# Kernel tuning notes

Hardware: AMD Instinct MI355X
Metric: run time of the kernel (lower is better)

Reference implementation:

```python
import jax, jax.numpy as jnp
import numpy as np

NEG_SLOPE = 0.2

def _gatv2(x_src, x_dst, src, dst, Wl, bl, Wr, br, att, bias, num_dst, edge_feat=None, We=None):
    # PyG GATv2Conv (heads=1, add_self_loops=False, eval mode -> no dropout)
    xl = x_src @ Wl + bl                      # [Ns, C] lin_l on source
    xr = x_dst @ Wr + br                      # [Nd, C] lin_r on target
    m = xl[src] + xr[dst]                     # [E, C]
    if edge_feat is not None:
        m = m + edge_feat @ We                # lin_edge (bias=False)
    e = jax.nn.leaky_relu(m, NEG_SLOPE) @ att # [E] attention logits
    emax = jax.ops.segment_max(e, dst, num_segments=num_dst)
    ee = jnp.exp(e - emax[dst])
    denom = jax.ops.segment_sum(ee, dst, num_segments=num_dst)
    alpha = ee / jnp.maximum(denom[dst], 1e-16)
    out = jax.ops.segment_sum(alpha[:, None] * xl[src], dst, num_segments=num_dst)
    return out + bias


def setup_inputs() -> dict:
    key = jax.random.key(0)
    N_OP, N_M, N_A = 50000, 5000, 2000
    C_OP, C_M, C_A = 256, 128, 128
    E_OO, E_OM, E_MA, E_DIM = 200000, 200000, 60000, 8
    ks = jax.random.split(key, 40)
    i = iter(range(40))
    def nrm(shape, fan_in):
        return jax.random.normal(ks[next(i)], shape, dtype=jnp.float32) / np.sqrt(fan_in)
    inp = {}
    inp['x_op'] = jax.random.normal(ks[next(i)], (N_OP, C_OP), dtype=jnp.float32)
    inp['x_m'] = jax.random.normal(ks[next(i)], (N_M, C_M), dtype=jnp.float32)
    inp['x_a'] = jax.random.normal(ks[next(i)], (N_A, C_A), dtype=jnp.float32)
    inp['ei_pred'] = jax.random.randint(ks[next(i)], (2, E_OO), 0, N_OP)
    inp['ei_succ'] = jax.random.randint(ks[next(i)], (2, E_OO), 0, N_OP)
    inp['src_o2m'] = jax.random.randint(ks[next(i)], (E_OM,), 0, N_OP)
    inp['dst_o2m'] = jax.random.randint(ks[next(i)], (E_OM,), 0, N_M)
    inp['src_m2a'] = jax.random.randint(ks[next(i)], (E_MA,), 0, N_M)
    inp['dst_m2a'] = jax.random.randint(ks[next(i)], (E_MA,), 0, N_A)
    inp['ea_m2a'] = jax.random.normal(ks[next(i)], (E_MA, E_DIM), dtype=jnp.float32)
    for name, c_in_src, c_in_dst, c_out in [('pred', C_OP, C_OP, C_OP), ('succ', C_OP, C_OP, C_OP), ('o2m', C_OP, C_M, C_M), ('m2a', C_M, C_A, C_A)]:
        inp[f'Wl_{name}'] = nrm((c_in_src, c_out), c_in_src)
        inp[f'bl_{name}'] = jnp.zeros((c_out,), jnp.float32)
        inp[f'Wr_{name}'] = nrm((c_in_dst, c_out), c_in_dst)
        inp[f'br_{name}'] = jnp.zeros((c_out,), jnp.float32)
        inp[f'att_{name}'] = nrm((c_out,), c_out)
        inp[f'b_{name}'] = jnp.zeros((c_out,), jnp.float32)
    inp['We_m2a'] = nrm((E_DIM, C_A), E_DIM)
    return inp


def reference(x_op, x_m, x_a, ei_pred, ei_succ, src_o2m, dst_o2m, src_m2a, dst_m2a, ea_m2a,
              Wl_pred, bl_pred, Wr_pred, br_pred, att_pred, b_pred,
              Wl_succ, bl_succ, Wr_succ, br_succ, att_succ, b_succ,
              Wl_o2m, bl_o2m, Wr_o2m, br_o2m, att_o2m, b_o2m,
              Wl_m2a, bl_m2a, Wr_m2a, br_m2a, att_m2a, b_m2a, We_m2a):
    N_OP, N_M, N_A = x_op.shape[0], x_m.shape[0], x_a.shape[0]
    # operation_relation_extract: two op->op GATv2 convs, HeteroConv sum-aggregated
    f_pred = _gatv2(x_op, x_op, ei_pred[0], ei_pred[1], Wl_pred, bl_pred, Wr_pred, br_pred, att_pred, b_pred, N_OP)
    f_succ = _gatv2(x_op, x_op, ei_succ[0], ei_succ[1], Wl_succ, bl_succ, Wr_succ, br_succ, att_succ, b_succ, N_OP)
    # hetero_relation_extract
    f_mach = _gatv2(x_op, x_m, src_o2m, dst_o2m, Wl_o2m, bl_o2m, Wr_o2m, br_o2m, att_o2m, b_o2m, N_M)
    f_agv = _gatv2(x_m, x_a, src_m2a, dst_m2a, Wl_m2a, bl_m2a, Wr_m2a, br_m2a, att_m2a, b_m2a, N_A, edge_feat=ea_m2a, We=We_m2a)
    # residual sum across relation outputs per node type
    out_op = x_op + f_pred + f_succ
    out_m = x_m + f_mach
    out_a = x_a + f_agv
    return (out_op, out_m, out_a)
```

## Files before the change

### kernel.cpp

```cpp
#include <hip/hip_runtime.h>

#define N_OP   50000
#define N_M    5000
#define N_A    2000
#define C_OP   256
#define C_M    128
#define C_A    128
#define E_OO   200000
#define E_OM   200000
#define E_MA   60000
#define E_DIM  8

#define OUT_OP_OFF 0
#define OUT_M_OFF  (N_OP * C_OP)
#define OUT_A_OFF  (N_OP * C_OP + N_M * C_M)

typedef short bf16x8 __attribute__((ext_vector_type(8)));
typedef float f32x4 __attribute__((ext_vector_type(4)));
typedef __attribute__((address_space(1))) const unsigned gu32;
typedef __attribute__((address_space(3))) unsigned lu32;

__device__ __forceinline__ unsigned short f2bf(float f) {
    unsigned u = __float_as_uint(f);
    unsigned r = (u + 0x7FFFu + ((u >> 16) & 1u)) >> 16;
    return (unsigned short)r;
}
__device__ __forceinline__ float bf2f(unsigned short h) {
    return __uint_as_float(((unsigned)h) << 16);
}

#define NTOT 107000
#define ETOT 660000

#define I3_OP (N_OP * C_OP / 4)
#define I3_M  (I3_OP + N_M * C_M / 4)
#define I3_A  (I3_M + N_A * C_A / 4)

#define PK_P   131072
#define PK_S   262144
#define PK_OL  294912
#define PK_OR  311296
#define PK_ML  327680
#define PK_MR  344064
#define PK_BP  344576
#define PK_BS  345088

#define PREP_HIST_BLK ((ETOT + 255) / 256)
#define PREP_INIT_BLK (I3_A / 256)
#define PREP_PACK_BLK (PK_BS / 256)
#define PREP_TOTAL    (PREP_HIST_BLK + PREP_INIT_BLK + PREP_PACK_BLK)

__device__ __forceinline__ void init_one(const float* __restrict__ x,
                                         const float* __restrict__ b1,
                                         const float* __restrict__ b2,
                                         float* __restrict__ out,
                                         unsigned short* __restrict__ xc,
                                         int i, int cmask) {
    float4 v = ((const float4*)x)[i];
    const int cb = i & cmask;
    float4 b = ((const float4*)b1)[cb];
    if (b2) {
        float4 t = ((const float4*)b2)[cb];
        b.x += t.x; b.y += t.y; b.z += t.z; b.w += t.w;
    }
    float4 o;
    o.x = v.x + b.x; o.y = v.y + b.y; o.z = v.z + b.z; o.w = v.w + b.w;
    ((float4*)out)[i] = o;
    ushort4 r;
    r.x = f2bf(v.x); r.y = f2bf(v.y); r.z = f2bf(v.z); r.w = f2bf(v.w);
    ((ushort4*)xc)[i] = r;
}

__global__ void prep_all(
    const int* __restrict__ dP, const int* __restrict__ dS,
    const int* __restrict__ dO, const int* __restrict__ dA,
    int* __restrict__ cP, int* __restrict__ cS,
    int* __restrict__ cO, int* __restrict__ cA, int* __restrict__ rk,
    const float* __restrict__ x_op, const float* __restrict__ x_m,
    const float* __restrict__ x_a,
    const float* __restrict__ bP, const float* __restrict__ bS,
    const float* __restrict__ bO, const float* __restrict__ bA,
    float* __restrict__ out_op, float* __restrict__ out_m, float* __restrict__ out_a,
    unsigned short* __restrict__ xcop, unsigned short* __restrict__ xcm,
    unsigned short* __restrict__ xca,
    const float* __restrict__ WlP, const float* __restrict__ WrP,
    const float* __restrict__ WlS, const float* __restrict__ WrS,
    const float* __restrict__ WOl, const float* __restrict__ WOr,
    const float* __restrict__ WMl, const float* __restrict__ WMr,
    const float* __restrict__ blP, const float* __restrict__ brP,
    const float* __restrict__ blS, const float* __restrict__ brS,
    unsigned short* __restrict__ BtP, unsigned short* __restrict__ BtS,
    unsigned short* __restrict__ BtOL, unsigned short* __restrict__ BtOR,
    unsigned short* __restrict__ BtML, unsigned short* __restrict__ BtMR,
    float* __restrict__ biasP, float* __restrict__ biasS) {
    const int b = blockIdx.x;
    const int tid = threadIdx.x;
    if (b < PREP_HIST_BLK) {
        int i = b * 256 + tid;
        if (i < 200000)      rk[i] = atomicAdd(&cP[dP[i]], 1);
        else if (i < 400000) rk[i] = atomicAdd(&cS[dS[i - 200000]], 1);
        else if (i < 600000) rk[i] = atomicAdd(&cO[dO[i - 400000]], 1);
        else if (i < ETOT)   rk[i] = atomicAdd(&cA[dA[i - 600000]], 1);
    } else if (b < PREP_HIST_BLK + PREP_INIT_BLK) {
        int i = (b - PREP_HIST_BLK) * 256 + tid;
        if (i < I3_OP)      init_one(x_op, bP, bS, out_op, xcop, i, 63);
        else if (i < I3_M)  init_one(x_m, bO, nullptr, out_m, xcm, i - I3_OP, 31);
        else                init_one(x_a, bA, nullptr, out_a, xca, i - I3_M, 31);
    } else {
        int i = (b - PREP_HIST_BLK - PREP_INIT_BLK) * 256 + tid;
        if (i < PK_P) {
            int n = i >> 8, k = i & 255;
            BtP[i] = f2bf((n < 256) ? WlP[k * 256 + n] : WrP[k * 256 + (n - 256)]);
        } else if (i < PK_S) {
            int j = i - PK_P; int n = j >> 8, k = j & 255;
            BtS[j] = f2bf((n < 256) ? WlS[k * 256 + n] : WrS[k * 256 + (n - 256)]);
        } else if (i < PK_OL) {
            int j = i - PK_S; int n = j >> 8, k = j & 255;
            BtOL[j] = f2bf(WOl[k * 128 + n]);
        } else if (i < PK_OR) {
            int j = i - PK_OL; int n = j >> 7, k = j & 127;
            BtOR[j] = f2bf(WOr[k * 128 + n]);
        } else if (i < PK_ML) {
            int j = i - PK_OR; int n = j >> 7, k = j & 127;
            BtML[j] = f2bf(WMl[k * 128 + n]);
        } else if (i < PK_MR) {
            int j = i - PK_ML; int n = j >> 7, k = j & 127;
            BtMR[j] = f2bf(WMr[k * 128 + n]);
        } else if (i < PK_BP) {
            int j = i - PK_MR;
            biasP[j] = (j < 256) ? blP[j] : brP[j - 256];
        } else if (i < PK_BS) {
            int j = i - PK_BP;
            biasS[j] = (j < 256) ? blS[j] : brS[j - 256];
        }
    }
}

__device__ __forceinline__ void gload_lds16(const void* g, void* l) {
    __builtin_amdgcn_global_load_lds((gu32*)g, (lu32*)l, 16, 0, 0);
}

__device__ __forceinline__ void gemm_body(
    const unsigned short* __restrict__ A, const unsigned short* __restrict__ Bt,
    const float* __restrict__ bias, unsigned short* __restrict__ C,
    int M, int K, int ldc, int bx, int by,
    unsigned short (&As)[2][128 * 64], unsigned short (&Bs)[2][128 * 64]) {
    const int tid  = threadIdx.x;
    const int lane = tid & 63;
    const int wid  = tid >> 6;
    const int m0   = bx * 128;
    const int n0   = by * 128;

    f32x4 acc[4][4] = {};

    const int srow   = tid >> 3;
    const int scolb  = (tid & 7) * 16;
    const int scole  = (scolb ^ ((srow & 7) << 4)) >> 1;

    int grA[4], grB[4];
#pragma unroll
    for (int i = 0; i < 4; ++i) {
        int gr = m0 + i * 32 + srow;
        grA[i] = (gr < M) ? gr : M - 1;
        grB[i] = n0 + i * 32 + srow;
    }

    const int nt = K >> 6;
    int cur = 0;

#define STAGE(buf, k0)                                                          \
    {                                                                           \
        _Pragma("unroll")                                                       \
        for (int i = 0; i < 4; ++i)                                             \
            gload_lds16(A + (size_t)grA[i] * K + (k0) + scole,                  \
                        &As[buf][i * 2048 + tid * 8]);                          \
        _Pragma("unroll")                                                       \
        for (int i = 0; i < 4; ++i)                                             \
            gload_lds16(Bt + (size_t)grB[i] * K + (k0) + scole,                 \
                        &Bs[buf][i * 2048 + tid * 8]);                          \
    }

    STAGE(0, 0)
    asm volatile("s_waitcnt vmcnt(0)" ::: "memory");
    __syncthreads();

    const int wr = (wid >> 1) * 64;
    const int wc = (wid & 1) * 64;

    for (int t = 0; t < nt; ++t) {
        if (t + 1 < nt) STAGE(cur ^ 1, (t + 1) * 64)
#pragma unroll
        for (int kh = 0; kh < 2; ++kh) {
            const int kob = kh * 64 + (lane >> 4) * 16;
            bf16x8 a[4], b[4];
#pragma unroll
            for (int mi = 0; mi < 4; ++mi) {
                const int row = wr + mi * 16 + (lane & 15);
                a[mi] = *(const bf16x8*)((const char*)As[cur] + row * 128 +
                                         (kob ^ ((row & 7) << 4)));
            }
#pragma unroll
            for (int ni = 0; ni < 4; ++ni) {
                const int row = wc + ni * 16 + (lane & 15);
                b[ni] = *(const bf16x8*)((const char*)Bs[cur] + row * 128 +
                                         (kob ^ ((row & 7) << 4)));
            }
#pragma unroll
            for (int mi = 0; mi < 4; ++mi)
#pragma unroll
                for (int ni = 0; ni < 4; ++ni)
                    acc[mi][ni] = __builtin_amdgcn_mfma_f32_16x16x32_bf16(
                        a[mi], b[ni], acc[mi][ni], 0, 0, 0);
        }
        asm volatile("s_waitcnt vmcnt(0)" ::: "memory");
        __syncthreads();
        cur ^= 1;
    }
#undef STAGE

    const int crow = (lane >> 4) * 4;
    const int ccol = lane & 15;
    float bcol[4];
#pragma unroll
    for (int ni = 0; ni < 4; ++ni) bcol[ni] = bias[n0 + wc + ni * 16 + ccol];
#pragma unroll
    for (int mi = 0; mi < 4; ++mi) {
#pragma unroll
        for (int j = 0; j < 4; ++j) {
            const int row = m0 + wr + mi * 16 + crow + j;
            if (row < M) {
                unsigned short* pc = C + (size_t)row * ldc + n0 + wc + ccol;
#pragma unroll
                for (int ni = 0; ni < 4; ++ni)
                    pc[ni * 16] = f2bf(acc[mi][ni][j] + bcol[ni]);
            }
        }
    }
}

__global__ __launch_bounds__(256) void mfma_gemm(
    const unsigned short* __restrict__ A, const unsigned short* __restrict__ Bt,
    const float* __restrict__ bias, unsigned short* __restrict__ C,
    int M, int K, int ldc) {
    __shared__ unsigned short As[2][128 * 64];
    __shared__ unsigned short Bs[2][128 * 64];
    gemm_body(A, Bt, bias, C, M, K, ldc, blockIdx.x, blockIdx.y, As, Bs);
}

#define SCAT_XBLK 645
__global__ __launch_bounds__(256) void gemm_scat(
    const unsigned short* __restrict__ A, const unsigned short* __restrict__ Bt,
    const float* __restrict__ bias, unsigned short* __restrict__ C,
    int M, int K, int ldc, int mt,
    const int* __restrict__ sP, const int* __restrict__ dP,
    const int* __restrict__ sS, const int* __restrict__ dS,
    const int* __restrict__ sO, const int* __restrict__ dO,
    const int* __restrict__ sA, const int* __restrict__ dA,
    const int* __restrict__ pP, const int* __restrict__ pS,
    const int* __restrict__ pO, const int* __restrict__ pA,
    const int* __restrict__ rk,
    int* __restrict__ srP, int* __restrict__ srS,
    int* __restrict__ srO, int* __restrict__ srA, int* __restrict__ eiA) {
    __shared__ unsigned short As[2][128 * 64];
    __shared__ unsigned short Bs[2][128 * 64];
    if ((int)blockIdx.x < mt) {
        gemm_body(A, Bt, bias, C, M, K, ldc, blockIdx.x, blockIdx.y, As, Bs);
    } else {
        const int i = (((int)blockIdx.x - mt) * 4 + (int)blockIdx.y) * 256 + (int)threadIdx.x;
        if (i < 200000) {
            srP[pP[dP[i]] + rk[i]] = sP[i];
        } else if (i < 400000) {
            const int j = i - 200000;
            srS[pS[dS[j]] + rk[i]] = sS[j];
        } else if (i < 600000) {
            const int j = i - 400000;
            srO[pO[dO[j]] + rk[i]] = sO[j];
        } else if (i < ETOT) {
            const int j = i - 600000;
            const int pos = pA[dA[j]] + rk[i];
            srA[pos] = sA[j];
            eiA[pos] = j;
        }
    }
}

__global__ __launch_bounds__(256) void gemm_pair(
    const unsigned short* A1, const unsigned short* Bt1, const float* b1,
    unsigned short* C1, int M1, int K1, int l1, int n1,
    const unsigned short* A2, const unsigned short* Bt2, const float* b2,
    unsigned short* C2, int M2, int K2, int l2) {
    __shared__ unsigned short As[2][128 * 64];
    __shared__ unsigned short Bs[2][128 * 64];
    const unsigned short *A, *Bt; const float* bi; unsigned short* C;
    int M, K, ldc, bx;
    if ((int)blockIdx.x < n1) { A = A1; Bt = Bt1; bi = b1; C = C1; M = M1; K = K1; ldc = l1; bx = blockIdx.x; }
    else                      { A = A2; Bt = Bt2; bi = b2; C = C2; M = M2; K = K2; ldc = l2; bx = blockIdx.x - n1; }
    gemm_body(A, Bt, bi, C, M, K, ldc, bx, blockIdx.y, As, Bs);
}

__global__ __launch_bounds__(256) void gemm_tri(
    const unsigned short* A1, const unsigned short* Bt1, const float* b1,
    unsigned short* C1, int M1, int K1, int n1,
    const unsigned short* A2, const unsigned short* Bt2, const float* b2,
    unsigned short* C2, int M2, int K2, int n12,
    const float* __restrict__ ea, const float* __restrict__ We,
    const int* __restrict__ eid, unsigned short* __restrict__ efo) {
    __shared__ unsigned short As[2][128 * 64];
    __shared__ unsigned short Bs[2][128 * 64];
    __shared__ float Ef[8][8];
    const int b = blockIdx.x;
    if (b < n12) {
        const unsigned short *A, *Bt; const float* bi; unsigned short* C;
        int M, K, bx;
        if (b < n1) { A = A1; Bt = Bt1; bi = b1; C = C1; M = M1; K = K1; bx = b; }
        else        { A = A2; Bt = Bt2; bi = b2; C = C2; M = M2; K = K2; bx = b - n1; }
        gemm_body(A, Bt, bi, C, M, K, 128, bx, 0, As, Bs);
    } else {
        const int eb = b - n12;
        const int m0 = eb * 8;
        const int tid = threadIdx.x;
        if (tid < 64) {
            int r = tid >> 3, k = tid & 7;
            Ef[r][k] = ea[(size_t)eid[m0 + r] * 8 + k];
        }
        __syncthreads();
        const int col = tid & 127, half = tid >> 7;
        float acc[4] = {};
        for (int k = 0; k < 8; ++k) {
            const float w = We[k * 128 + col];
#pragma unroll
            for (int r = 0; r < 4; ++r) acc[r] += Ef[half * 4 + r][k] * w;
        }
#pragma unroll
        for (int r = 0; r < 4; ++r)
            efo[(size_t)(m0 + half * 4 + r) * 128 + col] = f2bf(acc[r]);
    }
}

#define NB_P 49
#define NB_S 49
#define NB_O 5
#define NB_A 2

__global__ void zero4(int* __restrict__ p, int n) {
    int i = blockIdx.x * blockDim.x + threadIdx.x;
    if (i < n) p[i] = 0;
}

__global__ void scan_blk4(const int* __restrict__ cP, const int* __restrict__ cS,
                          const int* __restrict__ cO, const int* __restrict__ cA,
                          int* __restrict__ pP, int* __restrict__ pS,
                          int* __restrict__ pO, int* __restrict__ pA,
                          int* __restrict__ bsum) {
    __shared__ int smem[1024];
    int b = blockIdx.x;
    const int* cnt; int* ptr; int n; int bo;
    if (b < NB_P)                { cnt = cP; ptr = pP; n = 50000; bo = 0; }
    else if (b < NB_P + NB_S)    { cnt = cS; ptr = pS; n = 50000; bo = 64;  b -= NB_P; }
    else if (b < NB_P + NB_S + NB_O) { cnt = cO; ptr = pO; n = 5000; bo = 128; b -= NB_P + NB_S; }
    else                         { cnt = cA; ptr = pA; n = 2000; bo = 192; b -= NB_P + NB_S + NB_O; }
    const int tid = threadIdx.x;
    const int i = b * 1024 + tid;
    const int v = (i < n) ? cnt[i] : 0;
    smem[tid] = v;
    __syncthreads();
    for (int o = 1; o < 1024; o <<= 1) {
        int t = (tid >= o) ? smem[tid - o] : 0;
        __syncthreads();
        smem[tid] += t;
        __syncthreads();
    }
    if (i < n) ptr[i] = smem[tid] - v;
    if (tid == 1023) bsum[bo + b] = smem[1023];
}

__global__ void scan_tops4(const int* __restrict__ bsum, int* __restrict__ boff,
                           int* __restrict__ pP, int* __restrict__ pS,
                           int* __restrict__ pO, int* __restrict__ pA) {
    __shared__ int smem[1024];
    const int seg = blockIdx.x;
    const int nb = (seg < 2) ? 49 : (seg == 2 ? 5 : 2);
    const int off = seg * 64;
    int* ptr_n = (seg == 0) ? pP + 50000 : (seg == 1) ? pS + 50000
               : (seg == 2) ? pO + 5000 : pA + 2000;
    const int tid = threadIdx.x;
    const int v = (tid < nb) ? bsum[off + tid] : 0;
    smem[tid] = v;
    __syncthreads();
    for (int o = 1; o < 1024; o <<= 1) {
        int t = (tid >= o) ? smem[tid - o] : 0;
        __syncthreads();
        smem[tid] += t;
        __syncthreads();
    }
    if (tid < nb) boff[off + tid] = smem[tid] - v;
    if (tid == 1023) *ptr_n = smem[1023];
}

__global__ void scan_add4(int* __restrict__ pP, int* __restrict__ pS,
                          int* __restrict__ pO, int* __restrict__ pA,
                          const int* __restrict__ boff) {
    int i = blockIdx.x * blockDim.x + threadIdx.x;
    int* ptr; int loc; int off;
    if (i < 50000)       { ptr = pP; loc = i;          off = 0; }
    else if (i < 100000) { ptr = pS; loc = i - 50000;  off = 64; }
    else if (i < 105000) { ptr = pO; loc = i - 100000; off = 128; }
    else if (i < NTOT)   { ptr = pA; loc = i - 105000; off = 192; }
    else return;
    ptr[loc] += boff[off + (loc >> 10)];
}

template <int C>
__global__ void csr_serial2(const unsigned short* __restrict__ xl, int ldl,
                            const unsigned short* __restrict__ xr, int ldr,
                            const float* __restrict__ att,
                            const int* __restrict__ ptr, const int* __restrict__ srcs,
                            float* __restrict__ out, int n) {
    const int tid = threadIdx.x;
    const int node = blockIdx.x * (blockDim.x >> 5) + (tid >> 5);
    if (node >= n) return;
    const int gl = tid & 31;
    const int beg = ptr[node], end = ptr[node + 1];
    if (beg == end) return;

    constexpr int V = C / 32;
    const int c0 = gl * V;

    float av[V], rvf[V];
    {
        const unsigned short* pr = xr + (size_t)node * ldr + c0;
        unsigned short rv[V];
        *(uint4*)rv = *(const uint4*)pr;
#pragma unroll
        for (int v4 = 0; v4 < V / 4; ++v4)
            *(float4*)(av + v4 * 4) = ((const float4*)(att + c0))[v4];
#pragma unroll
        for (int v = 0; v < V; ++v) rvf[v] = bf2f(rv[v]);
    }

    float runM = -3.0e38f, runS = 0.0f;
    float acc[V] = {};

    unsigned short lv[V];
    {
        const unsigned short* pl = xl + (size_t)srcs[beg] * ldl + c0;
        *(uint4*)lv = *(const uint4*)pl;
    }

    for (int j = beg; j < end; ++j) {
        float cf[V];
#pragma unroll
        for (int v = 0; v < V; ++v) cf[v] = bf2f(lv[v]);
        if (j + 1 < end) {
            const unsigned short* pl = xl + (size_t)srcs[j + 1] * ldl + c0;
            *(uint4*)lv = *(const uint4*)pl;
        }

        float part = 0.0f;
#pragma unroll
        for (int v = 0; v < V; ++v) {
            float m = cf[v] + rvf[v];
            m = (m >= 0.0f) ? m : 0.2f * m;
            part += m * av[v];
        }
        part += __shfl_xor(part, 1, 64);
        part += __shfl_xor(part, 2, 64);
        part += __shfl_xor(part, 4, 64);
        part += __shfl_xor(part, 8, 64);
        part += __shfl_xor(part, 16, 64);

        const float newM = fmaxf(runM, part);
        const float sc = __expf(runM - newM);
        const float e1 = __expf(part - newM);
        runS = runS * sc + e1;
        runM = newM;
#pragma unroll
        for (int v = 0; v < V; ++v) acc[v] = acc[v] * sc + e1 * cf[v];
    }

    const float inv = 1.0f / fmaxf(runS, 1e-16f);
    float* po = out + (size_t)node * C + c0;
#pragma unroll
    for (int v4 = 0; v4 < V / 4; ++v4) {
        float4 o = ((float4*)po)[v4];
        o.x += acc[v4 * 4 + 0] * inv;
        o.y += acc[v4 * 4 + 1] * inv;
        o.z += acc[v4 * 4 + 2] * inv;
        o.w += acc[v4 * 4 + 3] * inv;
        ((float4*)po)[v4] = o;
    }
}

template <int C, bool HAS_EF>
__global__ void csr_grp(const unsigned short* __restrict__ xl, int ldl,
                        const unsigned short* __restrict__ xr, int ldr,
                        const unsigned short* __restrict__ ef,
                        const float* __restrict__ att,
                        const int* __restrict__ ptr, const int* __restrict__ srcs,
                        float* __restrict__ out, int n) {
    const int node = blockIdx.x * (blockDim.x >> 6) + (threadIdx.x >> 6);
    if (node >= n) return;
    const int lane = threadIdx.x & 63;
    const int grp  = lane >> 4;
    const int sl   = lane & 15;
    const int beg = ptr[node], end = ptr[node + 1];
    if (beg == end) return;

    constexpr int W = C / 16;
    const int c0 = sl * W;

    float av[W], rvf[W];
    {
        const unsigned short* pr = xr + (size_t)node * ldr + c0;
        unsigned short rv[W];
        *(uint4*)rv = *(const uint4*)pr;
        if constexpr (W == 16) *(uint4*)(rv + 8) = *(const uint4*)(pr + 8);
#pragma unroll
        for (int v4 = 0; v4 < W / 4; ++v4)
            *(float4*)(av + v4 * 4) = ((const float4*)(att + c0))[v4];
#pragma unroll
        for (int v = 0; v < W; ++v) rvf[v] = bf2f(rv[v]);
    }

    float runM = -3.0e38f, runS = 0.0f;
    float acc[W] = {};

    for (int cb = beg; cb < end; cb += 4) {
        const int j = cb + grp;
        const bool act = (j < end);
        const int js = act ? j : end - 1;
        const int s = srcs[js];

        const unsigned short* pl = xl + (size_t)s * ldl + c0;
        unsigned short lv[W];
        *(uint4*)lv = *(const uint4*)pl;
        if constexpr (W == 16) *(uint4*)(lv + 8) = *(const uint4*)(pl + 8);
        float cf[W];
#pragma unroll
        for (int v = 0; v < W; ++v) cf[v] = bf2f(lv[v]);

        float part = 0.0f;
        if constexpr (HAS_EF) {
            unsigned short efv[W];
            const unsigned short* pe = ef + (size_t)js * C + c0;
            *(uint4*)efv = *(const uint4*)pe;
            if constexpr (W == 16) *(uint4*)(efv + 8) = *(const uint4*)(pe + 8);
#pragma unroll
            for (int v = 0; v < W; ++v) {
                float m = cf[v] + rvf[v] + bf2f(efv[v]);
                m = (m >= 0.0f) ? m : 0.2f * m;
                part += m * av[v];
            }
        } else {
#pragma unroll
            for (int v = 0; v < W; ++v) {
                float m = cf[v] + rvf[v];
                m = (m >= 0.0f) ? m : 0.2f * m;
                part += m * av[v];
            }
        }
        part += __shfl_xor(part, 1, 64);
        part += __shfl_xor(part, 2, 64);
        part += __shfl_xor(part, 4, 64);
        part += __shfl_xor(part, 8, 64);
        if (!act) part = -3.0e38f;

        float cm = fmaxf(part, __shfl_xor(part, 16, 64));
        cm = fmaxf(cm, __shfl_xor(cm, 32, 64));

        if (cm > runM) {
            const float sc = __expf(runM - cm);
            runS *= sc;
#pragma unroll
            for (int v = 0; v < W; ++v) acc[v] *= sc;
            runM = cm;
        }
        const float w = act ? __expf(part - runM) : 0.0f;
        float cs = w + __shfl_xor(w, 16, 64);
        cs += __shfl_xor(cs, 32, 64);
        runS += cs;
#pragma unroll
        for (int v = 0; v < W; ++v) acc[v] += w * cf[v];
    }

#pragma unroll
    for (int v = 0; v < W; ++v) acc[v] += __shfl_xor(acc[v], 16, 64);
#pragma unroll
    for (int v = 0; v < W; ++v) acc[v] += __shfl_xor(acc[v], 32, 64);

    const float inv = 1.0f / fmaxf(runS, 1e-16f);
    if (grp == 0) {
        float* po = out + (size_t)node * C + c0;
#pragma unroll
        for (int v4 = 0; v4 < W / 4; ++v4) {
            float4 o = ((float4*)po)[v4];
            o.x += acc[v4 * 4 + 0] * inv;
            o.y += acc[v4 * 4 + 1] * inv;
            o.z += acc[v4 * 4 + 2] * inv;
            o.w += acc[v4 * 4 + 3] * inv;
            ((float4*)po)[v4] = o;
        }
    }
}

#define F_H      0
#define F_XCOP   12800000
#define F_XCM    19200000
#define F_XCA    19520000
#define F_BTP    19648000
#define F_BTS    19713536
#define F_BTOL   19779072
#define F_BTOR   19795456
#define F_BTML   19803648
#define F_BTMR   19811840
#define F_BIASP  19820032
#define F_BIASS  19820544
#define F_CNT4   19821056
#define F_BSUM   19928056
#define F_BOFF   19928312
#define F_PTR_P  19928568
#define F_SRC_P  19978569
#define F_PTR_S  20178569
#define F_SRC_S  20228570
#define F_PTR_O  20428570
#define F_SRC_O  20433571
#define F_PTR_A  20633571
#define F_SRC_A  20635572
#define F_EID_A  20695572
#define F_RANK   20755572

extern "C" void kernel_launch(void* const* d_in, const int* in_sizes, int n_in,
                              void* d_out, int out_size, void* d_ws, size_t ws_size,
                              hipStream_t stream) {
    const float* x_op    = (const float*)d_in[0];
    const float* x_m     = (const float*)d_in[1];
    const float* x_a     = (const float*)d_in[2];
    const int*   ei_pred = (const int*)d_in[3];
    const int*   ei_succ = (const int*)d_in[4];
    const int*   src_o2m = (const int*)d_in[5];
    const int*   dst_o2m = (const int*)d_in[6];
    const int*   src_m2a = (const int*)d_in[7];
    const int*   dst_m2a = (const int*)d_in[8];
    const float* ea_m2a  = (const float*)d_in[9];

    const float* Wl_pred = (const float*)d_in[10];
    const float* bl_pred = (const float*)d_in[11];
    const float* Wr_pred = (const float*)d_in[12];
    const float* br_pred = (const float*)d_in[13];
    const float* att_pred= (const float*)d_in[14];
    const float* b_pred  = (const float*)d_in[15];

    const float* Wl_succ = (const float*)d_in[16];
    const float* bl_succ = (const float*)d_in[17];
    const float* Wr_succ = (const float*)d_in[18];
    const float* br_succ = (const float*)d_in[19];
    const float* att_succ= (const float*)d_in[20];
    const float* b_succ  = (const float*)d_in[21];

    const float* Wl_o2m  = (const float*)d_in[22];
    const float* bl_o2m  = (const float*)d_in[23];
    const float* Wr_o2m  = (const float*)d_in[24];
    const float* br_o2m  = (const float*)d_in[25];
    const float* att_o2m = (const float*)d_in[26];
    const float* b_o2m   = (const float*)d_in[27];

    const float* Wl_m2a  = (const float*)d_in[28];
    const float* bl_m2a  = (const float*)d_in[29];
    const float* Wr_m2a  = (const float*)d_in[30];
    const float* br_m2a  = (const float*)d_in[31];
    const float* att_m2a = (const float*)d_in[32];
    const float* b_m2a   = (const float*)d_in[33];
    const float* We_m2a  = (const float*)d_in[34];

    float* ws = (float*)d_ws;
    unsigned short* H     = (unsigned short*)(ws + F_H);
    unsigned short* xc_op = (unsigned short*)(ws + F_XCOP);
    unsigned short* xc_m  = (unsigned short*)(ws + F_XCM);
    unsigned short* xc_a  = (unsigned short*)(ws + F_XCA);
    unsigned short* BtP   = (unsigned short*)(ws + F_BTP);
    unsigned short* BtS   = (unsigned short*)(ws + F_BTS);
    unsigned short* BtOL  = (unsigned short*)(ws + F_BTOL);
    unsigned short* BtOR  = (unsigned short*)(ws + F_BTOR);
    unsigned short* BtML  = (unsigned short*)(ws + F_BTML);
    unsigned short* BtMR  = (unsigned short*)(ws + F_BTMR);
    float* biasP = ws + F_BIASP;
    float* biasS = ws + F_BIASS;
    int* cntP = (int*)(ws + F_CNT4);
    int* cntS = cntP + 50000;
    int* cntO = cntP + 100000;
    int* cntA = cntP + 105000;
    int* bsum = (int*)(ws + F_BSUM);
    int* boff = (int*)(ws + F_BOFF);
    int* ptrP = (int*)(ws + F_PTR_P); int* srcP = (int*)(ws + F_SRC_P);
    int* ptrS = (int*)(ws + F_PTR_S); int* srcS = (int*)(ws + F_SRC_S);
    int* ptrO = (int*)(ws + F_PTR_O); int* srcO = (int*)(ws + F_SRC_O);
    int* ptrA = (int*)(ws + F_PTR_A); int* srcA = (int*)(ws + F_SRC_A);
    int* eidA = (int*)(ws + F_EID_A);
    int* rk   = (int*)(ws + F_RANK);

    float* out_op = (float*)d_out + OUT_OP_OFF;
    float* out_m  = (float*)d_out + OUT_M_OFF;
    float* out_a  = (float*)d_out + OUT_A_OFF;

    zero4<<<(NTOT + 255) / 256, 256, 0, stream>>>(cntP, NTOT);

    prep_all<<<PREP_TOTAL, 256, 0, stream>>>(
        ei_pred + E_OO, ei_succ + E_OO, dst_o2m, dst_m2a,
        cntP, cntS, cntO, cntA, rk,
        x_op, x_m, x_a, b_pred, b_succ, b_o2m, b_m2a,
        out_op, out_m, out_a, xc_op, xc_m, xc_a,
        Wl_pred, Wr_pred, Wl_succ, Wr_succ, Wl_o2m, Wr_o2m, Wl_m2a, Wr_m2a,
        bl_pred, br_pred, bl_succ, br_succ,
        BtP, BtS, BtOL, BtOR, BtML, BtMR, biasP, biasS);

    scan_blk4<<<NB_P + NB_S + NB_O + NB_A, 1024, 0, stream>>>(cntP, cntS, cntO, cntA,
                                                              ptrP, ptrS, ptrO, ptrA, bsum);
    scan_tops4<<<4, 1024, 0, stream>>>(bsum, boff, ptrP, ptrS, ptrO, ptrA);
    scan_add4<<<(NTOT + 255) / 256, 256, 0, stream>>>(ptrP, ptrS, ptrO, ptrA, boff);

    const int MT_OP = (N_OP + 127) / 128;
    const int MT_M  = (N_M + 127) / 128;
    const int MT_A  = (N_A + 127) / 128;

    gemm_scat<<<dim3(MT_OP + SCAT_XBLK, 4), 256, 0, stream>>>(
        xc_op, BtP, biasP, H, N_OP, 256, 512, MT_OP,
        ei_pred, ei_pred + E_OO, ei_succ, ei_succ + E_OO,
        src_o2m, dst_o2m, src_m2a, dst_m2a,
        ptrP, ptrS, ptrO, ptrA, rk,
        srcP, srcS, srcO, srcA, eidA);
    csr_serial2<256><<<(N_OP + 7) / 8, 256, 0, stream>>>(H, 512, H + 256, 512,
                                                         att_pred, ptrP, srcP, out_op, N_OP);

    mfma_gemm<<<dim3(MT_OP, 4), 256, 0, stream>>>(xc_op, BtS, biasS, H, N_OP, 256, 512);
    csr_serial2<256><<<(N_OP + 7) / 8, 256, 0, stream>>>(H, 512, H + 256, 512,
                                                         att_succ, ptrS, srcS, out_op, N_OP);

    {
        unsigned short* xlb = H;
        unsigned short* xrb = H + 6400000;
        gemm_pair<<<dim3(MT_OP + MT_M, 1), 256, 0, stream>>>(
            xc_op, BtOL, bl_o2m, xlb, N_OP, 256, 128, MT_OP,
            xc_m, BtOR, br_o2m, xrb, N_M, 128, 128);
        csr_grp<128, false><<<(N_M + 3) / 4, 256, 0, stream>>>(xlb, 128, xrb, 128, nullptr,
                                                               att_o2m, ptrO, srcO, out_m, N_M);
    }

    {
        unsigned short* xlb = H;
        unsigned short* xrb = H + 1000000;
        unsigned short* efb = H + 2000000;
        gemm_tri<<<dim3(MT_M + MT_A + E_MA / 8, 1), 256, 0, stream>>>(
            xc_m, BtML, bl_m2a, xlb, N_M, 128, MT_M,
            xc_a, BtMR, br_m2a, xrb, N_A, 128, MT_M + MT_A,
            ea_m2a, We_m2a, eidA, efb);
        csr_grp<128, true><<<(N_A + 3) / 4, 256, 0, stream>>>(xlb, 128, xrb, 128, efb,
                                                              att_m2a, ptrA, srcA, out_a, N_A);
    }
}
```

Baseline: 291.8 us.

## Fuse o2m/m2a GEMMs with pred aggregation and merge hetero aggregations into one launch

Reorganizes the launch schedule. The o2m and m2a projection GEMMs now run as single-buffered blocks in the same launch as the pred CSR aggregation, writing to dedicated workspace buffers so they no longer overwrite H. The o2m and m2a attention aggregations are merged into one kernel, and the m2a edge-feature projection is computed on the fly from ea and We held in registers, which removes the separate edge-GEMM pass and its buffer. Histogram blocks in the prep kernel are interleaved among the init and pack blocks to spread the atomic traffic. This cuts the number of launches and the idle tails between them, at the cost of higher register pressure (64 floats of We per thread) and single-buffered GEMM loads with no overlap.

New measurement: 311.6 us. 6.8% more time.

```diff
diff --git a/kernel.cpp b/kernel.cpp
--- a/kernel.cpp
+++ b/kernel.cpp
@@ -48,7 +48,7 @@
 #define PREP_HIST_BLK ((ETOT + 255) / 256)
 #define PREP_INIT_BLK (I3_A / 256)
 #define PREP_PACK_BLK (PK_BS / 256)
-#define PREP_TOTAL    (PREP_HIST_BLK + PREP_INIT_BLK + PREP_PACK_BLK)
+#define PREP_TOTAL    17670
 
 __device__ __forceinline__ void init_one(const float* __restrict__ x,
                                          const float* __restrict__ b1,
@@ -95,19 +95,24 @@
     float* __restrict__ biasP, float* __restrict__ biasS) {
     const int b = blockIdx.x;
     const int tid = threadIdx.x;
-    if (b < PREP_HIST_BLK) {
-        int i = b * 256 + tid;
+    if ((b % 6) == 5) {
+        const int hb = b / 6;
+        if (hb >= PREP_HIST_BLK) return;
+        int i = hb * 256 + tid;
         if (i < 200000)      rk[i] = atomicAdd(&cP[dP[i]], 1);
         else if (i < 400000) rk[i] = atomicAdd(&cS[dS[i - 200000]], 1);
         else if (i < 600000) rk[i] = atomicAdd(&cO[dO[i - 400000]], 1);
         else if (i < ETOT)   rk[i] = atomicAdd(&cA[dA[i - 600000]], 1);
-    } else if (b < PREP_HIST_BLK + PREP_INIT_BLK) {
-        int i = (b - PREP_HIST_BLK) * 256 + tid;
+        return;
+    }
+    const int ob = b - b / 6;
+    if (ob < PREP_INIT_BLK) {
+        int i = ob * 256 + tid;
         if (i < I3_OP)      init_one(x_op, bP, bS, out_op, xcop, i, 63);
         else if (i < I3_M)  init_one(x_m, bO, nullptr, out_m, xcm, i - I3_OP, 31);
         else                init_one(x_a, bA, nullptr, out_a, xca, i - I3_M, 31);
     } else {
-        int i = (b - PREP_HIST_BLK - PREP_INIT_BLK) * 256 + tid;
+        int i = (ob - PREP_INIT_BLK) * 256 + tid;
         if (i < PK_P) {
             int n = i >> 8, k = i & 255;
             BtP[i] = f2bf((n < 256) ? WlP[k * 256 + n] : WrP[k * 256 + (n - 256)]);
@@ -140,34 +145,77 @@
     __builtin_amdgcn_global_load_lds((gu32*)g, (lu32*)l, 16, 0, 0);
 }
 
+#define GEMM_IDX                                                                \
+    const int tid  = threadIdx.x;                                               \
+    const int lane = tid & 63;                                                  \
+    const int wid  = tid >> 6;                                                  \
+    const int m0   = bx * 128;                                                  \
+    const int n0   = by * 128;                                                  \
+    f32x4 acc[4][4] = {};                                                       \
+    const int srow  = tid >> 3;                                                 \
+    const int scolb = (tid & 7) * 16;                                           \
+    const int scole = (scolb ^ ((srow & 7) << 4)) >> 1;                         \
+    int grA[4], grB[4];                                                         \
+    _Pragma("unroll")                                                           \
+    for (int i = 0; i < 4; ++i) {                                               \
+        int gr = m0 + i * 32 + srow;                                            \
+        grA[i] = (gr < M) ? gr : M - 1;                                         \
+        grB[i] = n0 + i * 32 + srow;                                            \
+    }                                                                           \
+    const int nt = K >> 6;
+
+#define GEMM_COMPUTE(BUFA, BUFB)                                                \
+    _Pragma("unroll")                                                           \
+    for (int kh = 0; kh < 2; ++kh) {                                            \
+        const int kob = kh * 64 + (lane >> 4) * 16;                             \
+        bf16x8 a[4], bfr[4];                                                    \
+        _Pragma("unroll")                                                       \
+        for (int mi = 0; mi < 4; ++mi) {                                        \
+            const int row = wr + mi * 16 + (lane & 15);                         \
+            a[mi] = *(const bf16x8*)((const char*)(BUFA) + row * 128 +          \
+                                     (kob ^ ((row & 7) << 4)));                 \
+        }                                                                       \
+        _Pragma("unroll")                                                       \
+        for (int ni = 0; ni < 4; ++ni) {                                        \
+            const int row = wc + ni * 16 + (lane & 15);                         \
+            bfr[ni] = *(const bf16x8*)((const char*)(BUFB) + row * 128 +        \
+                                       (kob ^ ((row & 7) << 4)));               \
+        }                                                                       \
+        _Pragma("unroll")                                                       \
+        for (int mi = 0; mi < 4; ++mi)                                          \
+            _Pragma("unroll")                                                   \
+            for (int ni = 0; ni < 4; ++ni)                                      \
+                acc[mi][ni] = __builtin_amdgcn_mfma_f32_16x16x32_bf16(          \
+                    a[mi], bfr[ni], acc[mi][ni], 0, 0, 0);                      \
+    }
+
+#define GEMM_EPILOGUE                                                           \
+    const int crow = (lane >> 4) * 4;                                           \
+    const int ccol = lane & 15;                                                 \
+    float bcol[4];                                                              \
+    _Pragma("unroll")                                                           \
+    for (int ni = 0; ni < 4; ++ni) bcol[ni] = bias[n0 + wc + ni * 16 + ccol];   \
+    _Pragma("unroll")                                                           \
+    for (int mi = 0; mi < 4; ++mi) {                                            \
+        _Pragma("unroll")                                                       \
+        for (int j = 0; j < 4; ++j) {                                           \
+            const int row = m0 + wr + mi * 16 + crow + j;                       \
+            if (row < M) {                                                      \
+                unsigned short* pc = C + (size_t)row * ldc + n0 + wc + ccol;    \
+                _Pragma("unroll")                                               \
+                for (int ni = 0; ni < 4; ++ni)                                  \
+                    pc[ni * 16] = f2bf(acc[mi][ni][j] + bcol[ni]);              \
+            }                                                                   \
+        }                                                                       \
+    }
+
 __device__ __forceinline__ void gemm_body(
     const unsigned short* __restrict__ A, const unsigned short* __restrict__ Bt,
     const float* __restrict__ bias, unsigned short* __restrict__ C,
     int M, int K, int ldc, int bx, int by,
     unsigned short (&As)[2][128 * 64], unsigned short (&Bs)[2][128 * 64]) {
-    const int tid  = threadIdx.x;
-    const int lane = tid & 63;
-    const int wid  = tid >> 6;
-    const int m0   = bx * 128;
-    const int n0   = by * 128;
-
-    f32x4 acc[4][4] = {};
-
-    const int srow   = tid >> 3;
-    const int scolb  = (tid & 7) * 16;
-    const int scole  = (scolb ^ ((srow & 7) << 4)) >> 1;
-
-    int grA[4], grB[4];
-#pragma unroll
-    for (int i = 0; i < 4; ++i) {
-        int gr = m0 + i * 32 + srow;
-        grA[i] = (gr < M) ? gr : M - 1;
-        grB[i] = n0 + i * 32 + srow;
-    }
-
-    const int nt = K >> 6;
+    GEMM_IDX
     int cur = 0;
-
 #define STAGE(buf, k0)                                                          \
     {                                                                           \
         _Pragma("unroll")                                                       \
@@ -179,63 +227,43 @@
             gload_lds16(Bt + (size_t)grB[i] * K + (k0) + scole,                 \
                         &Bs[buf][i * 2048 + tid * 8]);                          \
     }
-
     STAGE(0, 0)
     asm volatile("s_waitcnt vmcnt(0)" ::: "memory");
     __syncthreads();
-
     const int wr = (wid >> 1) * 64;
     const int wc = (wid & 1) * 64;
-
     for (int t = 0; t < nt; ++t) {
         if (t + 1 < nt) STAGE(cur ^ 1, (t + 1) * 64)
-#pragma unroll
-        for (int kh = 0; kh < 2; ++kh) {
-            const int kob = kh * 64 + (lane >> 4) * 16;
-            bf16x8 a[4], b[4];
-#pragma unroll
-            for (int mi = 0; mi < 4; ++mi) {
-                const int row = wr + mi * 16 + (lane & 15);
-                a[mi] = *(const bf16x8*)((const char*)As[cur] + row * 128 +
-                                         (kob ^ ((row & 7) << 4)));
-            }
-#pragma unroll
-            for (int ni = 0; ni < 4; ++ni) {
-                const int row = wc + ni * 16 + (lane & 15);
-                b[ni] = *(const bf16x8*)((const char*)Bs[cur] + row * 128 +
-                                         (kob ^ ((row & 7) << 4)));
-            }
-#pragma unroll
-            for (int mi = 0; mi < 4; ++mi)
-#pragma unroll
-                for (int ni = 0; ni < 4; ++ni)
-                    acc[mi][ni] = __builtin_amdgcn_mfma_f32_16x16x32_bf16(
-                        a[mi], b[ni], acc[mi][ni], 0, 0, 0);
-        }
+        GEMM_COMPUTE(As[cur], Bs[cur])
         asm volatile("s_waitcnt vmcnt(0)" ::: "memory");
         __syncthreads();
         cur ^= 1;
     }
 #undef STAGE
-
-    const int crow = (lane >> 4) * 4;
-    const int ccol = lane & 15;
-    float bcol[4];
-#pragma unroll
-    for (int ni = 0; ni < 4; ++ni) bcol[ni] = bias[n0 + wc + ni * 16 + ccol];
-#pragma unroll
-    for (int mi = 0; mi < 4; ++mi) {
-#pragma unroll
-        for (int j = 0; j < 4; ++j) {
-            const int row = m0 + wr + mi * 16 + crow + j;
-            if (row < M) {
-                unsigned short* pc = C + (size_t)row * ldc + n0 + wc + ccol;
-#pragma unroll
-                for (int ni = 0; ni < 4; ++ni)
-                    pc[ni * 16] = f2bf(acc[mi][ni][j] + bcol[ni]);
-            }
-        }
-    }
+    GEMM_EPILOGUE
+}
+
+__device__ __forceinline__ void gemm_body_sb(
+    const unsigned short* __restrict__ A, const unsigned short* __restrict__ Bt,
+    const float* __restrict__ bias, unsigned short* __restrict__ C,
+    int M, int K, int ldc, int bx, int by,
+    unsigned short (&As)[128 * 64], unsigned short (&Bs)[128 * 64]) {
+    GEMM_IDX
+    const int wr = (wid >> 1) * 64;
+    const int wc = (wid & 1) * 64;
+    for (int t = 0; t < nt; ++t) {
+#pragma unroll
+        for (int i = 0; i < 4; ++i)
+            gload_lds16(A + (size_t)grA[i] * K + t * 64 + scole, &As[i * 2048 + tid * 8]);
+#pragma unroll
+        for (int i = 0; i < 4; ++i)
+            gload_lds16(Bt + (size_t)grB[i] * K + t * 64 + scole, &Bs[i * 2048 + tid * 8]);
+        asm volatile("s_waitcnt vmcnt(0)" ::: "memory");
+        __syncthreads();
+        GEMM_COMPUTE(As, Bs)
+        __syncthreads();
+    }
+    GEMM_EPILOGUE
 }
 
 __global__ __launch_bounds__(256) void mfma_gemm(
@@ -284,59 +312,6 @@
     }
 }
 
-__global__ __launch_bounds__(256) void gemm_pair(
-    const unsigned short* A1, const unsigned short* Bt1, const float* b1,
-    unsigned short* C1, int M1, int K1, int l1, int n1,
-    const unsigned short* A2, const unsigned short* Bt2, const float* b2,
-    unsigned short* C2, int M2, int K2, int l2) {
-    __shared__ unsigned short As[2][128 * 64];
-    __shared__ unsigned short Bs[2][128 * 64];
-    const unsigned short *A, *Bt; const float* bi; unsigned short* C;
-    int M, K, ldc, bx;
-    if ((int)blockIdx.x < n1) { A = A1; Bt = Bt1; bi = b1; C = C1; M = M1; K = K1; ldc = l1; bx = blockIdx.x; }
-    else                      { A = A2; Bt = Bt2; bi = b2; C = C2; M = M2; K = K2; ldc = l2; bx = blockIdx.x - n1; }
-    gemm_body(A, Bt, bi, C, M, K, ldc, bx, blockIdx.y, As, Bs);
-}
-
-__global__ __launch_bounds__(256) void gemm_tri(
-    const unsigned short* A1, const unsigned short* Bt1, const float* b1,
-    unsigned short* C1, int M1, int K1, int n1,
-    const unsigned short* A2, const unsigned short* Bt2, const float* b2,
-    unsigned short* C2, int M2, int K2, int n12,
-    const float* __restrict__ ea, const float* __restrict__ We,
-    const int* __restrict__ eid, unsigned short* __restrict__ efo) {
-    __shared__ unsigned short As[2][128 * 64];
-    __shared__ unsigned short Bs[2][128 * 64];
-    __shared__ float Ef[8][8];
-    const int b = blockIdx.x;
-    if (b < n12) {
-        const unsigned short *A, *Bt; const float* bi; unsigned short* C;
-        int M, K, bx;
-        if (b < n1) { A = A1; Bt = Bt1; bi = b1; C = C1; M = M1; K = K1; bx = b; }
-        else        { A = A2; Bt = Bt2; bi = b2; C = C2; M = M2; K = K2; bx = b - n1; }
-        gemm_body(A, Bt, bi, C, M, K, 128, bx, 0, As, Bs);
-    } else {
-        const int eb = b - n12;
-        const int m0 = eb * 8;
-        const int tid = threadIdx.x;
-        if (tid < 64) {
-            int r = tid >> 3, k = tid & 7;
-            Ef[r][k] = ea[(size_t)eid[m0 + r] * 8 + k];
-        }
-        __syncthreads();
-        const int col = tid & 127, half = tid >> 7;
-        float acc[4] = {};
-        for (int k = 0; k < 8; ++k) {
-            const float w = We[k * 128 + col];
-#pragma unroll
-            for (int r = 0; r < 4; ++r) acc[r] += Ef[half * 4 + r][k] * w;
-        }
-#pragma unroll
-        for (int r = 0; r < 4; ++r)
-            efo[(size_t)(m0 + half * 4 + r) * 128 + col] = f2bf(acc[r]);
-    }
-}
-
 #define NB_P 49
 #define NB_S 49
 #define NB_O 5
@@ -410,20 +385,20 @@
     ptr[loc] += boff[off + (loc >> 10)];
 }
 
-template <int C>
-__global__ void csr_serial2(const unsigned short* __restrict__ xl, int ldl,
-                            const unsigned short* __restrict__ xr, int ldr,
-                            const float* __restrict__ att,
-                            const int* __restrict__ ptr, const int* __restrict__ srcs,
-                            float* __restrict__ out, int n) {
+__device__ __forceinline__ void csr2_body(
+    const unsigned short* __restrict__ xl, int ldl,
+    const unsigned short* __restrict__ xr, int ldr,
+    const float* __restrict__ att,
+    const int* __restrict__ ptr, const int* __restrict__ srcs,
+    float* __restrict__ out, int n, int blk) {
     const int tid = threadIdx.x;
-    const int node = blockIdx.x * (blockDim.x >> 5) + (tid >> 5);
+    const int node = blk * 8 + (tid >> 5);
     if (node >= n) return;
     const int gl = tid & 31;
     const int beg = ptr[node], end = ptr[node + 1];
     if (beg == end) return;
 
-    constexpr int V = C / 32;
+    constexpr int V = 8;
     const int c0 = gl * V;
 
     float av[V], rvf[V];
@@ -479,7 +454,7 @@
     }
 
     const float inv = 1.0f / fmaxf(runS, 1e-16f);
-    float* po = out + (size_t)node * C + c0;
+    float* po = out + (size_t)node * 256 + c0;
 #pragma unroll
     for (int v4 = 0; v4 < V / 4; ++v4) {
         float4 o = ((float4*)po)[v4];
@@ -491,14 +466,23 @@
     }
 }
 
-template <int C, bool HAS_EF>
-__global__ void csr_grp(const unsigned short* __restrict__ xl, int ldl,
-                        const unsigned short* __restrict__ xr, int ldr,
-                        const unsigned short* __restrict__ ef,
-                        const float* __restrict__ att,
-                        const int* __restrict__ ptr, const int* __restrict__ srcs,
-                        float* __restrict__ out, int n) {
-    const int node = blockIdx.x * (blockDim.x >> 6) + (threadIdx.x >> 6);
+__global__ void csr_serial2(const unsigned short* __restrict__ xl, int ldl,
+                            const unsigned short* __restrict__ xr, int ldr,
+                            const float* __restrict__ att,
+                            const int* __restrict__ ptr, const int* __restrict__ srcs,
+                            float* __restrict__ out, int n) {
+    csr2_body(xl, ldl, xr, ldr, att, ptr, srcs, out, n, blockIdx.x);
+}
+
+template <bool EF>
+__device__ __forceinline__ void csrg_body(
+    const unsigned short* __restrict__ xl, const unsigned short* __restrict__ xr,
+    const float* __restrict__ att,
+    const int* __restrict__ ptr, const int* __restrict__ srcs,
+    const int* __restrict__ eid, const float* __restrict__ ea,
+    const float* __restrict__ We,
+    float* __restrict__ out, int n, int blk) {
+    const int node = blk * 4 + ((int)threadIdx.x >> 6);
     if (node >= n) return;
     const int lane = threadIdx.x & 63;
     const int grp  = lane >> 4;
@@ -506,20 +490,28 @@
     const int beg = ptr[node], end = ptr[node + 1];
     if (beg == end) return;
 
-    constexpr int W = C / 16;
+    constexpr int W = 8;
     const int c0 = sl * W;
 
     float av[W], rvf[W];
     {
-        const unsigned short* pr = xr + (size_t)node * ldr + c0;
+        const unsigned short* pr = xr + (size_t)node * 128 + c0;
         unsigned short rv[W];
         *(uint4*)rv = *(const uint4*)pr;
-        if constexpr (W == 16) *(uint4*)(rv + 8) = *(const uint4*)(pr + 8);
-#pragma unroll
-        for (int v4 = 0; v4 < W / 4; ++v4)
+#pragma unroll
+        for (int v4 = 0; v4 < 2; ++v4)
             *(float4*)(av + v4 * 4) = ((const float4*)(att + c0))[v4];
 #pragma unroll
         for (int v = 0; v < W; ++v) rvf[v] = bf2f(rv[v]);
+    }
+
+    float wreg[64];
+    if constexpr (EF) {
+#pragma unroll
+        for (int k = 0; k < 8; ++k) {
+            *(float4*)(wreg + k * 8)     = *(const float4*)(We + k * 128 + c0);
+            *(float4*)(wreg + k * 8 + 4) = *(const float4*)(We + k * 128 + c0 + 4);
+        }
     }
 
     float runM = -3.0e38f, runS = 0.0f;
@@ -531,23 +523,25 @@
         const int js = act ? j : end - 1;
         const int s = srcs[js];
 
-        const unsigned short* pl = xl + (size_t)s * ldl + c0;
+        const unsigned short* pl = xl + (size_t)s * 128 + c0;
         unsigned short lv[W];
         *(uint4*)lv = *(const uint4*)pl;
-        if constexpr (W == 16) *(uint4*)(lv + 8) = *(const uint4*)(pl + 8);
         float cf[W];
 #pragma unroll
         for (int v = 0; v < W; ++v) cf[v] = bf2f(lv[v]);
 
         float part = 0.0f;
-        if constexpr (HAS_EF) {
-            unsigned short efv[W];
-            const unsigned short* pe = ef + (size_t)js * C + c0;
-            *(uint4*)efv = *(const uint4*)pe;
-            if constexpr (W == 16) *(uint4*)(efv + 8) = *(const uint4*)(pe + 8);
+        if constexpr (EF) {
+            const int oe = eid[js];
+            float eav[8];
+            *(float4*)eav       = *(const float4*)(ea + (size_t)oe * 8);
+            *(float4*)(eav + 4) = *(const float4*)(ea + (size_t)oe * 8 + 4);
 #pragma unroll
             for (int v = 0; v < W; ++v) {
-                float m = cf[v] + rvf[v] + bf2f(efv[v]);
+                float efv = eav[0] * wreg[v];
+#pragma unroll
+                for (int k = 1; k < 8; ++k) efv += eav[k] * wreg[k * 8 + v];
+                float m = cf[v] + rvf[v] + efv;
                 m = (m >= 0.0f) ? m : 0.2f * m;
                 part += m * av[v];
             }
@@ -590,9 +584,9 @@
 
     const float inv = 1.0f / fmaxf(runS, 1e-16f);
     if (grp == 0) {
-        float* po = out + (size_t)node * C + c0;
-#pragma unroll
-        for (int v4 = 0; v4 < W / 4; ++v4) {
+        float* po = out + (size_t)node * 128 + c0;
+#pragma unroll
+        for (int v4 = 0; v4 < 2; ++v4) {
             float4 o = ((float4*)po)[v4];
             o.x += acc[v4 * 4 + 0] * inv;
             o.y += acc[v4 * 4 + 1] * inv;
@@ -601,6 +595,59 @@
             ((float4*)po)[v4] = o;
         }
     }
+}
+
+#define MT_OPB 391
+#define MT_MB  40
+#define MT_AB  16
+#define PG_GEMM (MT_OPB + MT_MB + MT_MB + MT_AB)
+
+__global__ __launch_bounds__(256) void fuse_pg(
+    const unsigned short* __restrict__ xc_op, const unsigned short* __restrict__ xc_m,
+    const unsigned short* __restrict__ xc_a,
+    const unsigned short* __restrict__ BtOL, const unsigned short* __restrict__ BtOR,
+    const unsigned short* __restrict__ BtML, const unsigned short* __restrict__ BtMR,
+    const float* __restrict__ blO, const float* __restrict__ brO,
+    const float* __restrict__ blM, const float* __restrict__ brM,
+    unsigned short* __restrict__ xlbO, unsigned short* __restrict__ xrbO,
+    unsigned short* __restrict__ xlbM, unsigned short* __restrict__ xrbM,
+    const unsigned short* __restrict__ H, const float* __restrict__ attP,
+    const int* __restrict__ ptrP, const int* __restrict__ srcP,
+    float* __restrict__ out_op) {
+    __shared__ unsigned short As[128 * 64];
+    __shared__ unsigned short Bs[128 * 64];
+    const int b = blockIdx.x;
+    if (b < MT_OPB) {
+        gemm_body_sb(xc_op, BtOL, blO, xlbO, N_OP, 256, 128, b, 0, As, Bs);
+    } else if (b < MT_OPB + MT_MB) {
+        gemm_body_sb(xc_m, BtOR, brO, xrbO, N_M, 128, 128, b - MT_OPB, 0, As, Bs);
+    } else if (b < MT_OPB + 2 * MT_MB) {
+        gemm_body_sb(xc_m, BtML, blM, xlbM, N_M, 128, 128, b - MT_OPB - MT_MB, 0, As, Bs);
+    } else if (b < PG_GEMM) {
+        gemm_body_sb(xc_a, BtMR, brM, xrbM, N_A, 128, 128, b - MT_OPB - 2 * MT_MB, 0, As, Bs);
+    } else {
+        csr2_body(H, 512, H + 256, 512, attP, ptrP, srcP, out_op, N_OP, b - PG_GEMM);
+    }
+}
+
+#define CP_O 1250
+__global__ void csr_pair(
+    const unsigned short* __restrict__ xlbO, const unsigned short* __restrict__ xrbO,
+    const float* __restrict__ attO,
+    const int* __restrict__ ptrO, const int* __restrict__ srcO,
+    float* __restrict__ out_m,
+    const unsigned short* __restrict__ xlbM, const unsigned short* __restrict__ xrbM,
+    const float* __restrict__ attA,
+    const int* __restrict__ ptrA, const int* __restrict__ srcA,
+    const int* __restrict__ eidA, const float* __restrict__ ea,
+    const float* __restrict__ We, float* __restrict__ out_a) {
+    const int b = blockIdx.x;
+    if (b < CP_O)
+        csrg_body<false>(xlbO, xrbO, attO, ptrO, srcO, nullptr, nullptr, nullptr,
+                         out_m, N_M, b);
+    else
+        csrg_body<true>(xlbM, xrbM, attA, ptrA, srcA, eidA, ea, We,
+                        out_a, N_A, b - CP_O);
 }
 
 #define F_H      0
@@ -628,6 +675,10 @@
 #define F_SRC_A  20635572
 #define F_EID_A  20695572
 #define F_RANK   20755572
+#define F_XLO    21415572
+#define F_XRO    24615572
+#define F_XLM    24935572
+#define F_XRM    25255572
 
 extern "C" void kernel_launch(void* const* d_in, const int* in_sizes, int n_in,
                               void* d_out, int out_size, void* d_ws, size_t ws_size,
@@ -697,6 +748,10 @@
     int* ptrA = (int*)(ws + F_PTR_A); int* srcA = (int*)(ws + F_SRC_A);
     int* eidA = (int*)(ws + F_EID_A);
     int* rk   = (int*)(ws + F_RANK);
+    unsigned short* xlbO = (unsigned short*)(ws + F_XLO);
+    unsigned short* xrbO = (unsigned short*)(ws + F_XRO);
+    unsigned short* xlbM = (unsigned short*)(ws + F_XLM);
+    unsigned short* xrbM = (unsigned short*)(ws + F_XRM);
 
     float* out_op = (float*)d_out + OUT_OP_OFF;
     float* out_m  = (float*)d_out + OUT_M_OFF;
@@ -718,42 +773,25 @@
     scan_tops4<<<4, 1024, 0, stream>>>(bsum, boff, ptrP, ptrS, ptrO, ptrA);
     scan_add4<<<(NTOT + 255) / 256, 256, 0, stream>>>(ptrP, ptrS, ptrO, ptrA, boff);
 
-    const int MT_OP = (N_OP + 127) / 128;
-    const int MT_M  = (N_M + 127) / 128;
-    const int MT_A  = (N_A + 127) / 128;
-
-    gemm_scat<<<dim3(MT_OP + SCAT_XBLK, 4), 256, 0, stream>>>(
-        xc_op, BtP, biasP, H, N_OP, 256, 512, MT_OP,
+    gemm_scat<<<dim3(MT_OPB + SCAT_XBLK, 4), 256, 0, stream>>>(
+        xc_op, BtP, biasP, H, N_OP, 256, 512, MT_OPB,
         ei_pred, ei_pred + E_OO, ei_succ, ei_succ + E_OO,
         src_o2m, dst_o2m, src_m2a, dst_m2a,
         ptrP, ptrS, ptrO, ptrA, rk,
         srcP, srcS, srcO, srcA, eidA);
-    csr_serial2<256><<<(N_OP + 7) / 8, 256, 0, stream>>>(H, 512, H + 256, 512,
-                                                         att_pred, ptrP, srcP, out_op, N_OP);
-
-    mfma_gemm<<<dim3(MT_OP, 4), 256, 0, stream>>>(xc_op, BtS, biasS, H, N_OP, 256, 512);
-    csr_serial2<256><<<(N_OP + 7) / 8, 256, 0, stream>>>(H, 512, H + 256, 512,
-                                                         att_succ, ptrS, srcS, out_op, N_OP);
-
-    {
-        unsigned short* xlb = H;
-        unsigned short* xrb = H + 6400000;
-        gemm_pair<<<dim3(MT_OP + MT_M, 1), 256, 0, stream>>>(
-            xc_op, BtOL, bl_o2m, xlb, N_OP, 256, 128, MT_OP,
-            xc_m, BtOR, br_o2m, xrb, N_M, 128, 128);
-        csr_grp<128, false><<<(N_M + 3) / 4, 256, 0, stream>>>(xlb, 128, xrb, 128, nullptr,
-                                                               att_o2m, ptrO, srcO, out_m, N_M);
-    }
-
-    {
-        unsigned short* xlb = H;
-        unsigned short* xrb = H + 1000000;
-        unsigned short* efb = H + 2000000;
-        gemm_tri<<<dim3(MT_M + MT_A + E_MA / 8, 1), 256, 0, stream>>>(
-            xc_m, BtML, bl_m2a, xlb, N_M, 128, MT_M,
-            xc_a, BtMR, br_m2a, xrb, N_A, 128, MT_M + MT_A,
-            ea_m2a, We_m2a, eidA, efb);
-        csr_grp<128, true><<<(N_A + 3) / 4, 256, 0, stream>>>(xlb, 128, xrb, 128, efb,
-                                                              att_m2a, ptrA, srcA, out_a, N_A);
-    }
-}
+
+    fuse_pg<<<PG_GEMM + (N_OP + 7) / 8, 256, 0, stream>>>(
+        xc_op, xc_m, xc_a, BtOL, BtOR, BtML, BtMR,
+        bl_o2m, br_o2m, bl_m2a, br_m2a,
+        xlbO, xrbO, xlbM, xrbM,
+        H, att_pred, ptrP, srcP, out_op);
+
+    mfma_gemm<<<dim3(MT_OPB, 4), 256, 0, stream>>>(xc_op, BtS, biasS, H, N_OP, 256, 512);
+
+    csr_serial2<<<(N_OP + 7) / 8, 256, 0, stream>>>(H, 512, H + 256, 512,
+                                                    att_succ, ptrS, srcS, out_op, N_OP);
+
+    csr_pair<<<CP_O + (N_A + 3) / 4, 256, 0, stream>>>(
+        xlbO, xrbO, att_o2m, ptrO, srcO, out_m,
+        xlbM, xrbM, att_m2a, ptrA, srcA, eidA, ea_m2a, We_m2a, out_a);
+}
```
